# Performance work log

Hardware: AMD Instinct MI355X
Metric: run time of the kernel (lower is better)

## Reference

```python
import jax, jax.numpy as jnp
import numpy as np

B, L, C, D, H, NB, K = 8, 1024, 4, 64, 8, 2, 16  # batch, seq, conds, dim, heads, blocks, rbf centers

def _ln(x, s, b):
    m = x.mean(-1, keepdims=True)
    v = x.var(-1, keepdims=True)
    return (x - m) / jnp.sqrt(v + 1e-6) * s + b

def setup_inputs() -> dict:
    key = jax.random.key(0)
    ks = jax.random.split(key, 24)
    rn = lambda i, shape, sc=0.02: jax.random.normal(ks[i], shape, jnp.float32) * sc
    inp = {}
    inp['z'] = jax.random.normal(ks[0], (B, L), jnp.float32)
    inp['conditionals'] = jax.random.normal(ks[1], (C,), jnp.float32)
    inp['s'] = jnp.sort(jax.random.uniform(ks[2], (L,), jnp.float32))
    inp['embed'] = rn(3, (L, 2 * D - (C + 1)))  # positional id embedding table
    # input MLP([4D, D]) with gelu
    inp['Win1'] = rn(4, (2 * D, 4 * D)); inp['bin1'] = jnp.zeros((4 * D,), jnp.float32)
    inp['Win2'] = rn(5, (4 * D, D));     inp['bin2'] = jnp.zeros((D,), jnp.float32)
    # per-block (leading dim NB) transformer params
    inp['ln1_s'] = jnp.ones((NB, D), jnp.float32); inp['ln1_b'] = jnp.zeros((NB, D), jnp.float32)
    inp['ln2_s'] = jnp.ones((NB, D), jnp.float32); inp['ln2_b'] = jnp.zeros((NB, D), jnp.float32)
    inp['Wq'] = rn(6, (NB, D, 2 * D)); inp['bq'] = jnp.zeros((NB, 2 * D), jnp.float32)
    inp['Wk'] = rn(7, (NB, D, 2 * D)); inp['bk'] = jnp.zeros((NB, 2 * D), jnp.float32)
    inp['Wv'] = rn(8, (NB, D, 2 * D)); inp['bv'] = jnp.zeros((NB, 2 * D), jnp.float32)
    inp['Wo'] = rn(9, (NB, 2 * D, D)); inp['bo'] = jnp.zeros((NB, D), jnp.float32)
    # RBF-network attention bias: features exp(-(d-c)^2/(2w^2)) -> linear to H heads
    inp['rbf_c'] = jnp.tile(jnp.linspace(-1.0, 1.0, K, dtype=jnp.float32)[None], (NB, 1))
    inp['rbf_logw'] = jnp.full((NB, K), -1.0, jnp.float32)
    inp['rbf_w'] = rn(10, (NB, K, H), 0.1); inp['rbf_b'] = jnp.zeros((NB, H), jnp.float32)
    # FFN MLP([4D, D])
    inp['W1'] = rn(11, (NB, D, 4 * D)); inp['b1'] = jnp.zeros((NB, 4 * D), jnp.float32)
    inp['W2'] = rn(12, (NB, 4 * D, D)); inp['b2'] = jnp.zeros((NB, D), jnp.float32)
    # head MLP([4D, D, 1])
    inp['Wh1'] = rn(13, (D, 4 * D)); inp['bh1'] = jnp.zeros((4 * D,), jnp.float32)
    inp['Wh2'] = rn(14, (4 * D, D)); inp['bh2'] = jnp.zeros((D,), jnp.float32)
    inp['Wh3'] = rn(15, (D, 1));     inp['bh3'] = jnp.zeros((1,), jnp.float32)
    return inp

def reference(z, conditionals, s, embed, Win1, bin1, Win2, bin2,
              ln1_s, ln1_b, ln2_s, ln2_b, Wq, bq, Wk, bk, Wv, bv, Wo, bo,
              rbf_c, rbf_logw, rbf_w, rbf_b, W1, b1, W2, b2,
              Wh1, bh1, Wh2, bh2, Wh3, bh3):
    Bn, Ln = z.shape
    Cn = conditionals.shape[0]
    Hn = rbf_w.shape[-1]
    dh = Wq.shape[-1] // Hn
    scale = 1.0 / jnp.sqrt(jnp.float32(dh))
    # cond_as_feats: [z, broadcast conditionals] -> (B, L, C+1); prepend ids embedding -> (B, L, 2D)
    feats = jnp.concatenate([
        jnp.broadcast_to(embed[None], (Bn,) + embed.shape),
        z[..., None],
        jnp.broadcast_to(conditionals[None, None, :], (Bn, Ln, Cn)),
    ], axis=-1)
    x = jax.nn.gelu(feats @ Win1 + bin1) @ Win2 + bin2  # (B, L, D)
    dist = s[:, None] - s[None, :]  # (L, L) pairwise query-key coordinate diff (same per batch)
    for i in range(Wq.shape[0]):
        h = _ln(x, ln1_s[i], ln1_b[i])
        q = (h @ Wq[i] + bq[i]).reshape(Bn, Ln, Hn, dh)
        k = (h @ Wk[i] + bk[i]).reshape(Bn, Ln, Hn, dh)
        v = (h @ Wv[i] + bv[i]).reshape(Bn, Ln, Hn, dh)
        scores = jnp.einsum('bqhd,bkhd->bhqk', q, k) * scale
        # RBF-network bias on pairwise distances, per head
        phi = jnp.exp(-(dist[..., None] - rbf_c[i]) ** 2 / (2.0 * jnp.exp(rbf_logw[i]) ** 2))  # (L, L, K)
        bias = jnp.einsum('qkf,fh->hqk', phi, rbf_w[i]) + rbf_b[i][:, None, None]  # (H, L, L)
        a = jax.nn.softmax(scores + bias[None], axis=-1)
        o = jnp.einsum('bhqk,bkhd->bqhd', a, v).reshape(Bn, Ln, Hn * dh)
        x = x + o @ Wo[i] + bo[i]
        h2 = _ln(x, ln2_s[i], ln2_b[i])
        x = x + jax.nn.gelu(h2 @ W1[i] + b1[i]) @ W2[i] + b2[i]
    hh = jax.nn.gelu(x @ Wh1 + bh1)
    hh = jax.nn.gelu(hh @ Wh2 + bh2)
    return hh @ Wh3 + bh3  # f_hat: (B, L, 1)
```

## Files before the change

### kernel.cpp

```cpp
#include <hip/hip_runtime.h>
#include <hip/hip_bf16.h>

#define BB   8
#define LL   1024
#define DD   64
#define D2   128
#define D4   256
#define HH   8
#define DH   16

typedef __attribute__((ext_vector_type(8))) short short8;
typedef __attribute__((ext_vector_type(4))) float floatx4;

#define LOG2E 1.4426950408889634f
#define QK_SEED -66.54214054f

#define OB_QUAR 1048576
#define L_QUAR  65536

#define OFF_WIN1   0
#define OFF_WIN2   65536
#define OFF_LAY0   98304
#define LAY_STRIDE 131072
#define OFF_WQ     0
#define OFF_WK     16384
#define OFF_WV     32768
#define OFF_WO     49152
#define OFF_W1     65536
#define OFF_W2     98304
#define OFF_WH1    360448
#define OFF_WH2    393216

__device__ __forceinline__ float gelu_tanh(float u) {
  float y = 0.7978845608028654f * (u + 0.044715f * u * u * u);
  return __fdividef(u, 1.0f + __expf(-2.0f * y));
}

__device__ __forceinline__ float wave_reduce_sum(float v) {
#pragma unroll
  for (int m = 32; m >= 1; m >>= 1) v += __shfl_xor(v, m, 64);
  return v;
}

__device__ __forceinline__ unsigned short f2bf(float x) {
  unsigned u = __float_as_uint(x);
  u += 0x7fffu + ((u >> 16) & 1u);
  return (unsigned short)(u >> 16);
}

__device__ __forceinline__ float bf2f(unsigned short x) {
  return __uint_as_float(((unsigned)x) << 16);
}

__device__ __forceinline__ void split_bf(float v, unsigned short& hi,
                                         unsigned short& lo) {
  hi = f2bf(v);
  lo = f2bf(v - bf2f(hi));
}

__device__ __forceinline__ unsigned pack_bf2(float a, float b) {
  unsigned ua = __float_as_uint(a) + 0x8000u;
  unsigned ub = __float_as_uint(b) + 0x8000u;
  return __builtin_amdgcn_perm(ub, ua, 0x07060302u);
}

__device__ __forceinline__ int frag_off(int k, int n, int K) {
  return (n >> 4) * (K * 16) + ((k >> 5) << 9) + (((k >> 3) & 3) << 7) +
         ((n & 15) << 3) + (k & 7);
}

template <int K, int KP>
__device__ __forceinline__ floatx4 mfma_tile(
    const unsigned short* Ah, const unsigned short* Al,
    const unsigned short* __restrict__ Bf, const unsigned short* __restrict__ Bfl,
    int lane, int lq, int quad, floatx4 C) {
  floatx4 C1 = {0.0f, 0.0f, 0.0f, 0.0f};
  floatx4 C2 = {0.0f, 0.0f, 0.0f, 0.0f};
#pragma unroll
  for (int kk = 0; kk < K; kk += 32) {
    short8 ah = *(const short8*)(Ah + lq * KP + kk + quad * 8);
    short8 al = *(const short8*)(Al + lq * KP + kk + quad * 8);
    short8 bh = *(const short8*)(Bf + (kk >> 5) * 512 + lane * 8);
    short8 bl = *(const short8*)(Bfl + (kk >> 5) * 512 + lane * 8);
    C  = __builtin_amdgcn_mfma_f32_16x16x32_bf16(ah, bh, C, 0, 0, 0);
    C1 = __builtin_amdgcn_mfma_f32_16x16x32_bf16(al, bh, C1, 0, 0, 0);
    C2 = __builtin_amdgcn_mfma_f32_16x16x32_bf16(ah, bl, C2, 0, 0, 0);
  }
#pragma unroll
  for (int r = 0; r < 4; ++r) C[r] += C1[r] + C2[r];
  return C;
}

struct PrepArgs {
  const float* src[16];
  int Kd[16], Nd[16], dst[16], elems[16];
};

__global__ __launch_bounds__(256) void k_prep_bias(
    PrepArgs a, unsigned short* __restrict__ arena,
    const float* __restrict__ s, const float* __restrict__ rbf_c,
    const float* __restrict__ rbf_logw, const float* __restrict__ rbf_w,
    const float* __restrict__ rbf_b, unsigned short* __restrict__ biasT) {
  int bid = blockIdx.x, t = threadIdx.x;
  if (bid < 2048) {
    int mid = bid >> 7;
    int e = (bid & 127) * 256 + t;
    int KN = a.elems[mid];
    if (e >= KN) return;
    int K = a.Kd[mid], N = a.Nd[mid];
    int n = e / K, k = e - n * K;
    float wv = a.src[mid][k * N + n];
    unsigned short hi, lo;
    split_bf(wv, hi, lo);
    int fo = frag_off(k, n, K);
    arena[a.dst[mid] + fo] = hi;
    arena[a.dst[mid] + KN + fo] = lo;
    return;
  }
  __shared__ float cs[16], iw[16];
  int rem = bid - 2048;
  int lay = rem >> 12;
  if (t < 16) {
    cs[t] = rbf_c[lay * 16 + t];
    iw[t] = 0.5f * __expf(-2.0f * rbf_logw[lay * 16 + t]);
  }
  __syncthreads();
  int id = (rem & 4095) * 256 + t;
  int q = id >> 10, k = id & 1023;
  float dd = s[q] - s[k];
  float acc[8];
#pragma unroll
  for (int h = 0; h < 8; ++h) acc[h] = rbf_b[lay * 8 + h];
#pragma unroll 1
  for (int f = 0; f < 16; ++f) {
    float e = dd - cs[f];
    float ph = __expf(-e * e * iw[f]);
#pragma unroll
    for (int h = 0; h < 8; ++h)
      acc[h] = fmaf(ph, rbf_w[lay * 128 + f * 8 + h], acc[h]);
  }
  unsigned short* bT = biasT + (size_t)lay * 8 * 1024 * 1024;
#pragma unroll
  for (int h = 0; h < 8; ++h)
    bT[(size_t)(h * 1024 + q) * 1024 + k] = f2bf(acc[h] * LOG2E);
}

__device__ __forceinline__ void qkv_tail(
    const float* xl, unsigned short* Sh, unsigned short* Sl,
    const unsigned short* __restrict__ arena, int lay,
    const float* __restrict__ ln_s, const float* __restrict__ ln_b,
    const float* __restrict__ bq, const float* __restrict__ bk,
    const float* __restrict__ bv, unsigned short* __restrict__ qo,
    unsigned short* __restrict__ ko, unsigned short* __restrict__ voT,
    int tok0, int t) {
  int w = t >> 6, lane = t & 63;
  int lq = lane & 15, quad = lane >> 4;
  float ss = ln_s[lay * 64 + lane], sb = ln_b[lay * 64 + lane];
#pragma unroll
  for (int tk = 0; tk < 4; ++tk) {
    int tok = w * 4 + tk;
    float v = xl[tok * 64 + lane];
    float s1 = v, s2 = v * v;
#pragma unroll
    for (int m = 32; m >= 1; m >>= 1) {
      s1 += __shfl_xor(s1, m, 64);
      s2 += __shfl_xor(s2, m, 64);
    }
    float mean = s1 * 0.015625f;
    float var = fmaf(-mean, mean, s2 * 0.015625f);
    float hv = (v - mean) * rsqrtf(var + 1e-6f) * ss + sb;
    unsigned short hi, lo;
    split_bf(hv, hi, lo);
    Sh[tok * 72 + lane] = hi;
    Sl[tok * 72 + lane] = lo;
  }
  __syncthreads();
  int b = tok0 >> 10, l0 = tok0 & 1023;
#pragma unroll 1
  for (int mat = 0; mat < 3; ++mat) {
    const unsigned short* Bh =
        arena + OFF_LAY0 + lay * LAY_STRIDE + mat * 16384;
    const unsigned short* Bl = Bh + 8192;
    const float* bias = (mat == 0 ? bq : mat == 1 ? bk : bv) + lay * 128;
#pragma unroll
    for (int j = 0; j < 2; ++j) {
      int tl = w + j * 4;
      int n = tl * 16 + lq;
      float bb = bias[n];
      floatx4 C = {bb, bb, bb, bb};
      C = mfma_tile<64, 72>(Sh, Sl, Bh + tl * 16 * 64, Bl + tl * 16 * 64,
                            lane, lq, quad, C);
      if (mat < 2) {
        unsigned short* outp = (mat == 0 ? qo : ko);
        size_t basea = ((size_t)(b * 8 + tl) * 1024 + l0 + quad * 4) * 16 + lq;
#pragma unroll
        for (int r = 0; r < 4; ++r)
          outp[basea + (size_t)r * 16] = f2bf(C[r]);
      } else {
        size_t basev = ((size_t)(b * 8 + tl) * 16 + lq) * 1024 + l0 + quad * 4;
#pragma unroll
        for (int r = 0; r < 4; ++r)
          voT[basev + r] = f2bf(C[r]);
      }
    }
  }
}

__global__ __launch_bounds__(256, 2) void k_in_qkv(
    const float* __restrict__ embed, const float* __restrict__ z,
    const float* __restrict__ cond, const unsigned short* __restrict__ arena,
    const float* __restrict__ bin1, const float* __restrict__ bin2,
    float* __restrict__ x, const float* __restrict__ ln1_s,
    const float* __restrict__ ln1_b, const float* __restrict__ bq,
    const float* __restrict__ bk, const float* __restrict__ bv,
    unsigned short* __restrict__ qo, unsigned short* __restrict__ ko,
    unsigned short* __restrict__ voT) {
  __shared__ __align__(16) unsigned short Ah[16 * 136], Al[16 * 136];
  __shared__ __align__(16) unsigned short Hh[16 * 264], Hl[16 * 264];
  __shared__ __align__(16) unsigned short Sh[16 * 72], Sl[16 * 72];
  __shared__ float xl[16 * 64];
  int t = threadIdx.x, w = t >> 6, lane = t & 63;
  int lq = lane & 15, quad = lane >> 4;
  int tok0 = blockIdx.x * 16;
  for (int idx = t; idx < 2048; idx += 256) {
    int tok = idx >> 7, dim = idx & 127;
    int bl = tok0 + tok, l = bl & (LL - 1);
    float v;
    if (dim < 123) v = embed[l * 123 + dim];
    else if (dim == 123) v = z[bl];
    else v = cond[dim - 124];
    unsigned short hi, lo;
    split_bf(v, hi, lo);
    Ah[tok * 136 + dim] = hi;
    Al[tok * 136 + dim] = lo;
  }
  __syncthreads();
  const unsigned short* B1h = arena + OFF_WIN1;
  const unsigned short* B1l = B1h + 32768;
#pragma unroll
  for (int j = 0; j < 4; ++j) {
    int tl = w * 4 + j, n = tl * 16 + lq;
    float bb = bin1[n];
    floatx4 C = {bb, bb, bb, bb};
    C = mfma_tile<128, 136>(Ah, Al, B1h + tl * 16 * 128, B1l + tl * 16 * 128,
                            lane, lq, quad, C);
#pragma unroll
    for (int r = 0; r < 4; ++r) {
      float g = gelu_tanh(C[r]);
      unsigned short hi, lo;
      split_bf(g, hi, lo);
      Hh[(quad * 4 + r) * 264 + n] = hi;
      Hl[(quad * 4 + r) * 264 + n] = lo;
    }
  }
  __syncthreads();
  const unsigned short* B2h = arena + OFF_WIN2;
  const unsigned short* B2l = B2h + 16384;
  {
    int n = w * 16 + lq;
    float bb = bin2[n];
    floatx4 C = {bb, bb, bb, bb};
    C = mfma_tile<256, 264>(Hh, Hl, B2h + w * 16 * 256, B2l + w * 16 * 256,
                            lane, lq, quad, C);
#pragma unroll
    for (int r = 0; r < 4; ++r) {
      int m = quad * 4 + r;
      x[(size_t)(tok0 + m) * 64 + n] = C[r];
      xl[m * 64 + n] = C[r];
    }
  }
  __syncthreads();
  qkv_tail(xl, Sh, Sl, arena, 0, ln1_s, ln1_b, bq, bk, bv,
           qo, ko, voT, tok0, t);
}

__global__ __launch_bounds__(256) void k_attn(
    const unsigned short* __restrict__ qg, const unsigned short* __restrict__ kg,
    const unsigned short* __restrict__ vgT, const unsigned short* __restrict__ biasT,
    float* __restrict__ og, float* __restrict__ lsum) {
  __shared__ __align__(16) unsigned short Kl[64 * 40];
  __shared__ __align__(16) unsigned short VT[16 * 72];
  __shared__ __align__(16) unsigned short Pl[4][16 * 72];
  __shared__ __align__(16) unsigned short Bch[64 * 72];
  int t = threadIdx.x, w = t >> 6, lane = t & 63;
  int lq = lane & 15, quad = lane >> 4;
  int bid = blockIdx.x;
  int quarter = bid >> 10;
  int rem = bid & 1023;
  int b = rem >> 7, h = (rem >> 4) & 7, qblk = rem & 15;
  int q0w = qblk * 64 + w * 16;
  int kbase = quarter * 256;
  size_t bh = (size_t)(b * 8 + h) * 1024;
  size_t bh16 = (size_t)(b * 8 + h) * 16;

  ((uint4*)Kl)[t] = uint4{0, 0, 0, 0};
  if (t < 64) ((uint4*)Kl)[256 + t] = uint4{0, 0, 0, 0};

  short8 Qb = {};
  if (quad < 2)
    Qb = *(const short8*)(qg + (bh + q0w + lq) * 16 + quad * 8);

  float l = 0.0f;
  floatx4 O = {0.0f, 0.0f, 0.0f, 0.0f};

  int key = t >> 2, dp = (t & 3) * 4;
  int drow = t >> 4, vcol = (t & 15) * 4;
  int qrow = t >> 2, bcol = (t & 3) * 16;
  const unsigned short* kgp = kg + (bh + kbase + key) * 16 + dp;
  const unsigned short* vgp = vgT + (bh16 + drow) * 1024 + kbase + vcol;
  const unsigned short* bgp =
      biasT + ((size_t)(h * 1024 + qblk * 64 + qrow)) * 1024 + kbase + bcol;

  uint2 kpre = *(const uint2*)(kgp);
  uint2 vpre = *(const uint2*)(vgp);
  uint4 bpre0 = *(const uint4*)(bgp);
  uint4 bpre1 = *(const uint4*)(bgp + 8);

#pragma unroll 1
  for (int kc = 0; kc < 256; kc += 64) {
    __syncthreads();
    *(uint2*)(Kl + key * 40 + dp) = kpre;
    *(uint2*)(VT + drow * 72 + vcol) = vpre;
    *(uint4*)(Bch + qrow * 72 + bcol) = bpre0;
    *(uint4*)(Bch + qrow * 72 + bcol + 8) = bpre1;
    __syncthreads();
    if (kc + 64 < 256) {
      kpre = *(const uint2*)(kgp + (size_t)(kc + 64) * 16);
      vpre = *(const uint2*)(vgp + (kc + 64));
      bpre0 = *(const uint4*)(bgp + (kc + 64));
      bpre1 = *(const uint4*)(bgp + (kc + 64) + 8);
    }
    float psum = 0.0f;
    unsigned short* pw = &Pl[w][lq * 72];
#pragma unroll
    for (int tile = 0; tile < 4; ++tile) {
      short8 A = *(const short8*)(Kl + (tile * 16 + lq) * 40 + quad * 8);
      floatx4 c = {QK_SEED, QK_SEED, QK_SEED, QK_SEED};
      c = __builtin_amdgcn_mfma_f32_16x16x32_bf16(A, Qb, c, 0, 0, 0);
      ushort4 bb = *(const ushort4*)(Bch + (w * 16 + lq) * 72 +
                                     tile * 16 + quad * 4);
      float p0 = exp2f(fmaf(c[0], 0.25f * LOG2E, bf2f(bb.x)));
      float p1 = exp2f(fmaf(c[1], 0.25f * LOG2E, bf2f(bb.y)));
      float p2 = exp2f(fmaf(c[2], 0.25f * LOG2E, bf2f(bb.z)));
      float p3 = exp2f(fmaf(c[3], 0.25f * LOG2E, bf2f(bb.w)));
      psum += (p0 + p1) + (p2 + p3);
      uint2 pk;
      pk.x = pack_bf2(p0, p1);
      pk.y = pack_bf2(p2, p3);
      *(uint2*)(pw + tile * 16 + quad * 4) = pk;
    }
    psum += __shfl_xor(psum, 16, 64);
    psum += __shfl_xor(psum, 32, 64);
    l += psum;
    asm volatile("s_waitcnt lgkmcnt(0)" ::: "memory");
#pragma unroll
    for (int i = 0; i < 2; ++i) {
      short8 Pa = *(const short8*)(pw + i * 32 + quad * 8);
      short8 Vb = *(const short8*)(&VT[lq * 72 + i * 32 + quad * 8]);
      O = __builtin_amdgcn_mfma_f32_16x16x32_bf16(Pa, Vb, O, 0, 0, 0);
    }
  }
  float* ogh = og + (size_t)quarter * OB_QUAR;
#pragma unroll
  for (int r = 0; r < 4; ++r)
    ogh[((size_t)(b * 1024 + q0w + quad * 4 + r)) * 128 + h * 16 + lq] = O[r];
  if (quad == 0)
    lsum[(size_t)quarter * L_QUAR + (size_t)(b * 1024 + q0w + lq) * 8 + h] = l;
}

__device__ __forceinline__ void pf_body(
    const float* __restrict__ ob, const float* __restrict__ lsum,
    const unsigned short* __restrict__ arena,
    const float* __restrict__ bo, float* __restrict__ x,
    const float* __restrict__ ln_s, const float* __restrict__ ln_b,
    const float* __restrict__ b1, const float* __restrict__ b2, int lay,
    unsigned short* Ah, unsigned short* Al, unsigned short* Sh,
    unsigned short* Sl, unsigned short* Hh, unsigned short* Hl, float* xl,
    int tok0, int t, bool write_x) {
  int w = t >> 6, lane = t & 63;
  int lq = lane & 15, quad = lane >> 4;
  const unsigned short* labase = arena + OFF_LAY0 + lay * LAY_STRIDE;
  const float* ob1 = ob + OB_QUAR;
  const float* ob2 = ob + 2 * OB_QUAR;
  const float* ob3 = ob + 3 * OB_QUAR;
  for (int idx = t * 4; idx < 2048; idx += 1024) {
    int row = idx >> 7, col = idx & 127;
    int hh = col >> 4;
    int tok = tok0 + row;
    float lv = ((lsum[(size_t)tok * 8 + hh] +
                 lsum[L_QUAR + (size_t)tok * 8 + hh]) +
                (lsum[2 * L_QUAR + (size_t)tok * 8 + hh] +
                 lsum[3 * L_QUAR + (size_t)tok * 8 + hh]));
    float linv = 1.0f / lv;
    float4 v0 = *(const float4*)(ob + (size_t)tok * 128 + col);
    float4 v1 = *(const float4*)(ob1 + (size_t)tok * 128 + col);
    float4 v2 = *(const float4*)(ob2 + (size_t)tok * 128 + col);
    float4 v3 = *(const float4*)(ob3 + (size_t)tok * 128 + col);
    float4 v;
    v.x = ((v0.x + v1.x) + (v2.x + v3.x)) * linv;
    v.y = ((v0.y + v1.y) + (v2.y + v3.y)) * linv;
    v.z = ((v0.z + v1.z) + (v2.z + v3.z)) * linv;
    v.w = ((v0.w + v1.w) + (v2.w + v3.w)) * linv;
    unsigned short h0, e0, h1, e1, h2, e2, h3, e3;
    split_bf(v.x, h0, e0); split_bf(v.y, h1, e1);
    split_bf(v.z, h2, e2); split_bf(v.w, h3, e3);
    unsigned* ph = (unsigned*)(Ah + row * 136 + col);
    ph[0] = (unsigned)h0 | ((unsigned)h1 << 16);
    ph[1] = (unsigned)h2 | ((unsigned)h3 << 16);
    unsigned* pl = (unsigned*)(Al + row * 136 + col);
    pl[0] = (unsigned)e0 | ((unsigned)e1 << 16);
    pl[1] = (unsigned)e2 | ((unsigned)e3 << 16);
  }
  __syncthreads();
  {
    const unsigned short* Bh = labase + OFF_WO;
    const unsigned short* Bl = Bh + 8192;
    int n = w * 16 + lq;
    float bb = bo[lay * 64 + n];
    floatx4 C = {bb, bb, bb, bb};
    C = mfma_tile<128, 136>(Ah, Al, Bh + w * 16 * 128, Bl + w * 16 * 128,
                            lane, lq, quad, C);
#pragma unroll
    for (int r = 0; r < 4; ++r) {
      int m = quad * 4 + r;
      xl[m * 64 + n] = x[(size_t)(tok0 + m) * 64 + n] + C[r];
    }
  }
  __syncthreads();
  {
    float ss = ln_s[lay * 64 + lane], sb = ln_b[lay * 64 + lane];
#pragma unroll
    for (int tk = 0; tk < 4; ++tk) {
      int tok = w * 4 + tk;
      float v = xl[tok * 64 + lane];
      float s1 = v, s2 = v * v;
#pragma unroll
      for (int m = 32; m >= 1; m >>= 1) {
        s1 += __shfl_xor(s1, m, 64);
        s2 += __shfl_xor(s2, m, 64);
      }
      float mean = s1 * 0.015625f;
      float var = fmaf(-mean, mean, s2 * 0.015625f);
      float hv = (v - mean) * rsqrtf(var + 1e-6f) * ss + sb;
      unsigned short hi, lo;
      split_bf(hv, hi, lo);
      Sh[tok * 72 + lane] = hi;
      Sl[tok * 72 + lane] = lo;
    }
  }
  __syncthreads();
  {
    const unsigned short* Bh = labase + OFF_W1;
    const unsigned short* Bl = Bh + 16384;
#pragma unroll
    for (int j = 0; j < 4; ++j) {
      int tl = w * 4 + j, n = tl * 16 + lq;
      float bb = b1[lay * 256 + n];
      floatx4 C = {bb, bb, bb, bb};
      C = mfma_tile<64, 72>(Sh, Sl, Bh + tl * 16 * 64, Bl + tl * 16 * 64,
                            lane, lq, quad, C);
#pragma unroll
      for (int r = 0; r < 4; ++r) {
        float g = gelu_tanh(C[r]);
        unsigned short hi, lo;
        split_bf(g, hi, lo);
        Hh[(quad * 4 + r) * 264 + n] = hi;
        Hl[(quad * 4 + r) * 264 + n] = lo;
      }
    }
  }
  __syncthreads();
  {
    const unsigned short* Bh = labase + OFF_W2;
    const unsigned short* Bl = Bh + 16384;
    int n = w * 16 + lq;
    float bb = b2[lay * 64 + n];
    floatx4 C = {bb, bb, bb, bb};
    C = mfma_tile<256, 264>(Hh, Hl, Bh + w * 16 * 256, Bl + w * 16 * 256,
                            lane, lq, quad, C);
#pragma unroll
    for (int r = 0; r < 4; ++r) {
      int m = quad * 4 + r;
      float xv = xl[m * 64 + n] + C[r];
      xl[m * 64 + n] = xv;
      if (write_x) x[(size_t)(tok0 + m) * 64 + n] = xv;
    }
  }
  __syncthreads();
}

__global__ __launch_bounds__(256, 2) void k_pf_qkv(
    const float* __restrict__ ob, const float* __restrict__ lsum,
    const unsigned short* __restrict__ arena,
    const float* __restrict__ bo, float* __restrict__ x,
    const float* __restrict__ ln2_s, const float* __restrict__ ln2_b,
    const float* __restrict__ b1, const float* __restrict__ b2, int lay,
    const float* __restrict__ ln1_s, const float* __restrict__ ln1_b,
    const float* __restrict__ bq, const float* __restrict__ bk,
    const float* __restrict__ bv, unsigned short* __restrict__ qo,
    unsigned short* __restrict__ ko, unsigned short* __restrict__ voT) {
  __shared__ __align__(16) unsigned short Ah[16 * 136], Al[16 * 136];
  __shared__ __align__(16) unsigned short Sh[16 * 72], Sl[16 * 72];
  __shared__ __align__(16) unsigned short Hh[16 * 264], Hl[16 * 264];
  __shared__ float xl[16 * 64];
  int t = threadIdx.x;
  int tok0 = blockIdx.x * 16;
  pf_body(ob, lsum, arena, bo, x, ln2_s, ln2_b, b1, b2, lay,
          Ah, Al, Sh, Sl, Hh, Hl, xl, tok0, t, true);
  qkv_tail(xl, Sh, Sl, arena, lay + 1, ln1_s, ln1_b, bq, bk, bv,
           qo, ko, voT, tok0, t);
}

__global__ __launch_bounds__(256, 2) void k_pf_head(
    const float* __restrict__ ob, const float* __restrict__ lsum,
    const unsigned short* __restrict__ arena,
    const float* __restrict__ bo, float* __restrict__ x,
    const float* __restrict__ ln2_s, const float* __restrict__ ln2_b,
    const float* __restrict__ b1, const float* __restrict__ b2, int lay,
    const float* __restrict__ bh1, const float* __restrict__ bh2,
    const float* __restrict__ Wh3, const float* __restrict__ bh3,
    float* __restrict__ out) {
  __shared__ __align__(16) unsigned short Ah[16 * 136], Al[16 * 136];
  __shared__ __align__(16) unsigned short Sh[16 * 72], Sl[16 * 72];
  __shared__ __align__(16) unsigned short Hh[16 * 264], Hl[16 * 264];
  __shared__ float xl[16 * 64];
  int t = threadIdx.x, w = t >> 6, lane = t & 63;
  int lq = lane & 15, quad = lane >> 4;
  int tok0 = blockIdx.x * 16;
  pf_body(ob, lsum, arena, bo, x, ln2_s, ln2_b, b1, b2, lay,
          Ah, Al, Sh, Sl, Hh, Hl, xl, tok0, t, false);
#pragma unroll
  for (int tk = 0; tk < 4; ++tk) {
    int tok = w * 4 + tk;
    unsigned short hi, lo;
    split_bf(xl[tok * 64 + lane], hi, lo);
    Sh[tok * 72 + lane] = hi;
    Sl[tok * 72 + lane] = lo;
  }
  __syncthreads();
  {
    const unsigned short* Bh = arena + OFF_WH1;
    const unsigned short* Bl = Bh + 16384;
#pragma unroll
    for (int j = 0; j < 4; ++j) {
      int tl = w * 4 + j, n = tl * 16 + lq;
      float bb = bh1[n];
      floatx4 C = {bb, bb, bb, bb};
      C = mfma_tile<64, 72>(Sh, Sl, Bh + tl * 16 * 64, Bl + tl * 16 * 64,
                            lane, lq, quad, C);
#pragma unroll
      for (int r = 0; r < 4; ++r) {
        float g = gelu_tanh(C[r]);
        unsigned short hi, lo;
        split_bf(g, hi, lo);
        Hh[(quad * 4 + r) * 264 + n] = hi;
        Hl[(quad * 4 + r) * 264 + n] = lo;
      }
    }
  }
  __syncthreads();
  {
    const unsigned short* Bh = arena + OFF_WH2;
    const unsigned short* Bl = Bh + 16384;
    int n = w * 16 + lq;
    float bb = bh2[n];
    floatx4 C = {bb, bb, bb, bb};
    C = mfma_tile<256, 264>(Hh, Hl, Bh + w * 16 * 256, Bl + w * 16 * 256,
                            lane, lq, quad, C);
    __syncthreads();
#pragma unroll
    for (int r = 0; r < 4; ++r)
      xl[(quad * 4 + r) * 64 + n] = gelu_tanh(C[r]);
  }
  __syncthreads();
  float wv3 = Wh3[lane];
#pragma unroll
  for (int tk = 0; tk < 4; ++tk) {
    int tok = w * 4 + tk;
    float v = xl[tok * 64 + lane] * wv3;
    float sum = wave_reduce_sum(v);
    if (lane == 0) out[tok0 + tok] = sum + bh3[0];
  }
}

extern "C" void kernel_launch(void* const* d_in, const int* in_sizes, int n_in,
                              void* d_out, int out_size, void* d_ws, size_t ws_size,
                              hipStream_t stream) {
  const float* z      = (const float*)d_in[0];
  const float* cond   = (const float*)d_in[1];
  const float* s      = (const float*)d_in[2];
  const float* embed  = (const float*)d_in[3];
  const float* Win1   = (const float*)d_in[4];
  const float* bin1   = (const float*)d_in[5];
  const float* Win2   = (const float*)d_in[6];
  const float* bin2   = (const float*)d_in[7];
  const float* ln1_s  = (const float*)d_in[8];
  const float* ln1_b  = (const float*)d_in[9];
  const float* ln2_s  = (const float*)d_in[10];
  const float* ln2_b  = (const float*)d_in[11];
  const float* Wq     = (const float*)d_in[12];
  const float* bq     = (const float*)d_in[13];
  const float* Wk     = (const float*)d_in[14];
  const float* bk     = (const float*)d_in[15];
  const float* Wv     = (const float*)d_in[16];
  const float* bv     = (const float*)d_in[17];
  const float* Wo     = (const float*)d_in[18];
  const float* bo     = (const float*)d_in[19];
  const float* rbf_c  = (const float*)d_in[20];
  const float* rbf_lw = (const float*)d_in[21];
  const float* rbf_w  = (const float*)d_in[22];
  const float* rbf_b  = (const float*)d_in[23];
  const float* W1     = (const float*)d_in[24];
  const float* b1     = (const float*)d_in[25];
  const float* W2     = (const float*)d_in[26];
  const float* b2     = (const float*)d_in[27];
  const float* Wh1    = (const float*)d_in[28];
  const float* bh1    = (const float*)d_in[29];
  const float* Wh2    = (const float*)d_in[30];
  const float* bh2    = (const float*)d_in[31];
  const float* Wh3    = (const float*)d_in[32];
  const float* bh3    = (const float*)d_in[33];

  char* base = (char*)d_ws;
  float*          x     = (float*)(base);
  unsigned short* qb    = (unsigned short*)(base + (2u << 20));
  unsigned short* kb    = (unsigned short*)(base + (4u << 20));
  unsigned short* vbT   = (unsigned short*)(base + (6u << 20));
  float*          ob    = (float*)(base + (8u << 20));
  float*          lsum  = (float*)(base + (24u << 20));
  unsigned short* biasT = (unsigned short*)(base + (25u << 20));
  unsigned short* arena = (unsigned short*)(base + (57u << 20));

  PrepArgs pa;
  auto set = [&](int i, const float* sp, int K, int N, int dst) {
    pa.src[i] = sp; pa.Kd[i] = K; pa.Nd[i] = N; pa.dst[i] = dst;
    pa.elems[i] = K * N;
  };
  set(0, Win1, 128, 256, OFF_WIN1);
  set(1, Win2, 256, 64, OFF_WIN2);
  for (int lay = 0; lay < 2; ++lay) {
    int lb = OFF_LAY0 + lay * LAY_STRIDE;
    set(2 + lay * 6, Wq + lay * 8192, 64, 128, lb + OFF_WQ);
    set(3 + lay * 6, Wk + lay * 8192, 64, 128, lb + OFF_WK);
    set(4 + lay * 6, Wv + lay * 8192, 64, 128, lb + OFF_WV);
    set(5 + lay * 6, Wo + lay * 8192, 128, 64, lb + OFF_WO);
    set(6 + lay * 6, W1 + lay * 16384, 64, 256, lb + OFF_W1);
    set(7 + lay * 6, W2 + lay * 16384, 256, 64, lb + OFF_W2);
  }
  set(14, Wh1, 64, 256, OFF_WH1);
  set(15, Wh2, 256, 64, OFF_WH2);

  k_prep_bias<<<2048 + 8192, 256, 0, stream>>>(pa, arena, s, rbf_c, rbf_lw,
                                               rbf_w, rbf_b, biasT);
  k_in_qkv<<<512, 256, 0, stream>>>(embed, z, cond, arena, bin1, bin2, x,
                                    ln1_s, ln1_b, bq, bk, bv, qb, kb, vbT);
  k_attn<<<4096, 256, 0, stream>>>(qb, kb, vbT, biasT, ob, lsum);
  k_pf_qkv<<<512, 256, 0, stream>>>(ob, lsum, arena, bo, x, ln2_s, ln2_b,
                                    b1, b2, 0, ln1_s, ln1_b, bq, bk, bv,
                                    qb, kb, vbT);
  k_attn<<<4096, 256, 0, stream>>>(qb, kb, vbT,
                                   biasT + (size_t)8 * 1024 * 1024, ob, lsum);
  k_pf_head<<<512, 256, 0, stream>>>(ob, lsum, arena, bo, x, ln2_s, ln2_b,
                                     b1, b2, 1, bh1, bh2, Wh3, bh3,
                                     (float*)d_out);
}
```

Baseline: 238.6 us.

## Double threads per block in MLP kernels with split-K reduction via LDS

Result: no change. 239.3 us (median of 2 runs) (+0.3%).

```diff
diff --git a/kernel.cpp b/kernel.cpp
--- a/kernel.cpp
+++ b/kernel.cpp
@@ -157,8 +157,8 @@
   int lq = lane & 15, quad = lane >> 4;
   float ss = ln_s[lay * 64 + lane], sb = ln_b[lay * 64 + lane];
 #pragma unroll
-  for (int tk = 0; tk < 4; ++tk) {
-    int tok = w * 4 + tk;
+  for (int tk = 0; tk < 2; ++tk) {
+    int tok = w * 2 + tk;
     float v = xl[tok * 64 + lane];
     float s1 = v, s2 = v * v;
 #pragma unroll
@@ -176,37 +176,34 @@
   }
   __syncthreads();
   int b = tok0 >> 10, l0 = tok0 & 1023;
+  int tl = w;
 #pragma unroll 1
   for (int mat = 0; mat < 3; ++mat) {
     const unsigned short* Bh =
         arena + OFF_LAY0 + lay * LAY_STRIDE + mat * 16384;
     const unsigned short* Bl = Bh + 8192;
     const float* bias = (mat == 0 ? bq : mat == 1 ? bk : bv) + lay * 128;
-#pragma unroll
-    for (int j = 0; j < 2; ++j) {
-      int tl = w + j * 4;
-      int n = tl * 16 + lq;
-      float bb = bias[n];
-      floatx4 C = {bb, bb, bb, bb};
-      C = mfma_tile<64, 72>(Sh, Sl, Bh + tl * 16 * 64, Bl + tl * 16 * 64,
-                            lane, lq, quad, C);
-      if (mat < 2) {
-        unsigned short* outp = (mat == 0 ? qo : ko);
-        size_t basea = ((size_t)(b * 8 + tl) * 1024 + l0 + quad * 4) * 16 + lq;
-#pragma unroll
-        for (int r = 0; r < 4; ++r)
-          outp[basea + (size_t)r * 16] = f2bf(C[r]);
-      } else {
-        size_t basev = ((size_t)(b * 8 + tl) * 16 + lq) * 1024 + l0 + quad * 4;
-#pragma unroll
-        for (int r = 0; r < 4; ++r)
-          voT[basev + r] = f2bf(C[r]);
-      }
-    }
-  }
-}
-
-__global__ __launch_bounds__(256, 2) void k_in_qkv(
+    int n = tl * 16 + lq;
+    float bb = bias[n];
+    floatx4 C = {bb, bb, bb, bb};
+    C = mfma_tile<64, 72>(Sh, Sl, Bh + tl * 16 * 64, Bl + tl * 16 * 64,
+                          lane, lq, quad, C);
+    if (mat < 2) {
+      unsigned short* outp = (mat == 0 ? qo : ko);
+      size_t basea = ((size_t)(b * 8 + tl) * 1024 + l0 + quad * 4) * 16 + lq;
+#pragma unroll
+      for (int r = 0; r < 4; ++r)
+        outp[basea + (size_t)r * 16] = f2bf(C[r]);
+    } else {
+      size_t basev = ((size_t)(b * 8 + tl) * 16 + lq) * 1024 + l0 + quad * 4;
+#pragma unroll
+      for (int r = 0; r < 4; ++r)
+        voT[basev + r] = f2bf(C[r]);
+    }
+  }
+}
+
+__global__ __launch_bounds__(512, 4) void k_in_qkv(
     const float* __restrict__ embed, const float* __restrict__ z,
     const float* __restrict__ cond, const unsigned short* __restrict__ arena,
     const float* __restrict__ bin1, const float* __restrict__ bin2,
@@ -219,10 +216,11 @@
   __shared__ __align__(16) unsigned short Hh[16 * 264], Hl[16 * 264];
   __shared__ __align__(16) unsigned short Sh[16 * 72], Sl[16 * 72];
   __shared__ float xl[16 * 64];
+  __shared__ __align__(16) float red[4 * 64 * 4];
   int t = threadIdx.x, w = t >> 6, lane = t & 63;
   int lq = lane & 15, quad = lane >> 4;
   int tok0 = blockIdx.x * 16;
-  for (int idx = t; idx < 2048; idx += 256) {
+  for (int idx = t; idx < 2048; idx += 512) {
     int tok = idx >> 7, dim = idx & 127;
     int bl = tok0 + tok, l = bl & (LL - 1);
     float v;
@@ -238,8 +236,8 @@
   const unsigned short* B1h = arena + OFF_WIN1;
   const unsigned short* B1l = B1h + 32768;
 #pragma unroll
-  for (int j = 0; j < 4; ++j) {
-    int tl = w * 4 + j, n = tl * 16 + lq;
+  for (int j = 0; j < 2; ++j) {
+    int tl = w * 2 + j, n = tl * 16 + lq;
     float bb = bin1[n];
     floatx4 C = {bb, bb, bb, bb};
     C = mfma_tile<128, 136>(Ah, Al, B1h + tl * 16 * 128, B1l + tl * 16 * 128,
@@ -254,19 +252,31 @@
     }
   }
   __syncthreads();
-  const unsigned short* B2h = arena + OFF_WIN2;
-  const unsigned short* B2l = B2h + 16384;
   {
-    int n = w * 16 + lq;
-    float bb = bin2[n];
-    floatx4 C = {bb, bb, bb, bb};
-    C = mfma_tile<256, 264>(Hh, Hl, B2h + w * 16 * 256, B2l + w * 16 * 256,
+    const unsigned short* B2h = arena + OFF_WIN2;
+    const unsigned short* B2l = B2h + 16384;
+    int tile = w & 3, kh = w >> 2, koff = kh * 128;
+    int n = tile * 16 + lq;
+    floatx4 C = {0.0f, 0.0f, 0.0f, 0.0f};
+    if (kh == 0) {
+      float bb = bin2[n];
+      C[0] = bb; C[1] = bb; C[2] = bb; C[3] = bb;
+    }
+    C = mfma_tile<128, 264>(Hh + koff, Hl + koff,
+                            B2h + tile * 16 * 256 + (koff >> 5) * 512,
+                            B2l + tile * 16 * 256 + (koff >> 5) * 512,
                             lane, lq, quad, C);
-#pragma unroll
-    for (int r = 0; r < 4; ++r) {
-      int m = quad * 4 + r;
-      x[(size_t)(tok0 + m) * 64 + n] = C[r];
-      xl[m * 64 + n] = C[r];
+    if (kh) *(floatx4*)&red[(tile * 64 + lane) * 4] = C;
+    __syncthreads();
+    if (!kh) {
+      floatx4 Cp = *(const floatx4*)&red[(tile * 64 + lane) * 4];
+#pragma unroll
+      for (int r = 0; r < 4; ++r) {
+        int m = quad * 4 + r;
+        float cv = C[r] + Cp[r];
+        x[(size_t)(tok0 + m) * 64 + n] = cv;
+        xl[m * 64 + n] = cv;
+      }
     }
   }
   __syncthreads();
@@ -376,14 +386,15 @@
     const float* __restrict__ b1, const float* __restrict__ b2, int lay,
     unsigned short* Ah, unsigned short* Al, unsigned short* Sh,
     unsigned short* Sl, unsigned short* Hh, unsigned short* Hl, float* xl,
-    int tok0, int t, bool write_x) {
+    float* red, int tok0, int t, bool write_x) {
   int w = t >> 6, lane = t & 63;
   int lq = lane & 15, quad = lane >> 4;
   const unsigned short* labase = arena + OFF_LAY0 + lay * LAY_STRIDE;
   const float* ob1 = ob + OB_QUAR;
   const float* ob2 = ob + 2 * OB_QUAR;
   const float* ob3 = ob + 3 * OB_QUAR;
-  for (int idx = t * 4; idx < 2048; idx += 1024) {
+  {
+    int idx = t * 4;
     int row = idx >> 7, col = idx & 127;
     int hh = col >> 4;
     int tok = tok0 + row;
@@ -415,23 +426,34 @@
   {
     const unsigned short* Bh = labase + OFF_WO;
     const unsigned short* Bl = Bh + 8192;
-    int n = w * 16 + lq;
-    float bb = bo[lay * 64 + n];
-    floatx4 C = {bb, bb, bb, bb};
-    C = mfma_tile<128, 136>(Ah, Al, Bh + w * 16 * 128, Bl + w * 16 * 128,
-                            lane, lq, quad, C);
-#pragma unroll
-    for (int r = 0; r < 4; ++r) {
-      int m = quad * 4 + r;
-      xl[m * 64 + n] = x[(size_t)(tok0 + m) * 64 + n] + C[r];
+    int tile = w & 3, kh = w >> 2, koff = kh * 64;
+    int n = tile * 16 + lq;
+    floatx4 C = {0.0f, 0.0f, 0.0f, 0.0f};
+    if (kh == 0) {
+      float bb = bo[lay * 64 + n];
+      C[0] = bb; C[1] = bb; C[2] = bb; C[3] = bb;
+    }
+    C = mfma_tile<64, 136>(Ah + koff, Al + koff,
+                           Bh + tile * 16 * 128 + (koff >> 5) * 512,
+                           Bl + tile * 16 * 128 + (koff >> 5) * 512,
+                           lane, lq, quad, C);
+    if (kh) *(floatx4*)&red[(tile * 64 + lane) * 4] = C;
+    __syncthreads();
+    if (!kh) {
+      floatx4 Cp = *(const floatx4*)&red[(tile * 64 + lane) * 4];
+#pragma unroll
+      for (int r = 0; r < 4; ++r) {
+        int m = quad * 4 + r;
+        xl[m * 64 + n] = x[(size_t)(tok0 + m) * 64 + n] + C[r] + Cp[r];
+      }
     }
   }
   __syncthreads();
   {
     float ss = ln_s[lay * 64 + lane], sb = ln_b[lay * 64 + lane];
 #pragma unroll
-    for (int tk = 0; tk < 4; ++tk) {
-      int tok = w * 4 + tk;
+    for (int tk = 0; tk < 2; ++tk) {
+      int tok = w * 2 + tk;
       float v = xl[tok * 64 + lane];
       float s1 = v, s2 = v * v;
 #pragma unroll
@@ -453,8 +475,8 @@
     const unsigned short* Bh = labase + OFF_W1;
     const unsigned short* Bl = Bh + 16384;
 #pragma unroll
-    for (int j = 0; j < 4; ++j) {
-      int tl = w * 4 + j, n = tl * 16 + lq;
+    for (int j = 0; j < 2; ++j) {
+      int tl = w * 2 + j, n = tl * 16 + lq;
       float bb = b1[lay * 256 + n];
       floatx4 C = {bb, bb, bb, bb};
       C = mfma_tile<64, 72>(Sh, Sl, Bh + tl * 16 * 64, Bl + tl * 16 * 64,
@@ -473,23 +495,34 @@
   {
     const unsigned short* Bh = labase + OFF_W2;
     const unsigned short* Bl = Bh + 16384;
-    int n = w * 16 + lq;
-    float bb = b2[lay * 64 + n];
-    floatx4 C = {bb, bb, bb, bb};
-    C = mfma_tile<256, 264>(Hh, Hl, Bh + w * 16 * 256, Bl + w * 16 * 256,
+    int tile = w & 3, kh = w >> 2, koff = kh * 128;
+    int n = tile * 16 + lq;
+    floatx4 C = {0.0f, 0.0f, 0.0f, 0.0f};
+    if (kh == 0) {
+      float bb = b2[lay * 64 + n];
+      C[0] = bb; C[1] = bb; C[2] = bb; C[3] = bb;
+    }
+    C = mfma_tile<128, 264>(Hh + koff, Hl + koff,
+                            Bh + tile * 16 * 256 + (koff >> 5) * 512,
+                            Bl + tile * 16 * 256 + (koff >> 5) * 512,
                             lane, lq, quad, C);
-#pragma unroll
-    for (int r = 0; r < 4; ++r) {
-      int m = quad * 4 + r;
-      float xv = xl[m * 64 + n] + C[r];
-      xl[m * 64 + n] = xv;
-      if (write_x) x[(size_t)(tok0 + m) * 64 + n] = xv;
-    }
-  }
-  __syncthreads();
-}
-
-__global__ __launch_bounds__(256, 2) void k_pf_qkv(
+    if (kh) *(floatx4*)&red[(tile * 64 + lane) * 4] = C;
+    __syncthreads();
+    if (!kh) {
+      floatx4 Cp = *(const floatx4*)&red[(tile * 64 + lane) * 4];
+#pragma unroll
+      for (int r = 0; r < 4; ++r) {
+        int m = quad * 4 + r;
+        float xv = xl[m * 64 + n] + C[r] + Cp[r];
+        xl[m * 64 + n] = xv;
+        if (write_x) x[(size_t)(tok0 + m) * 64 + n] = xv;
+      }
+    }
+  }
+  __syncthreads();
+}
+
+__global__ __launch_bounds__(512, 4) void k_pf_qkv(
     const float* __restrict__ ob, const float* __restrict__ lsum,
     const unsigned short* __restrict__ arena,
     const float* __restrict__ bo, float* __restrict__ x,
@@ -503,15 +536,16 @@
   __shared__ __align__(16) unsigned short Sh[16 * 72], Sl[16 * 72];
   __shared__ __align__(16) unsigned short Hh[16 * 264], Hl[16 * 264];
   __shared__ float xl[16 * 64];
+  __shared__ __align__(16) float red[4 * 64 * 4];
   int t = threadIdx.x;
   int tok0 = blockIdx.x * 16;
   pf_body(ob, lsum, arena, bo, x, ln2_s, ln2_b, b1, b2, lay,
-          Ah, Al, Sh, Sl, Hh, Hl, xl, tok0, t, true);
+          Ah, Al, Sh, Sl, Hh, Hl, xl, red, tok0, t, true);
   qkv_tail(xl, Sh, Sl, arena, lay + 1, ln1_s, ln1_b, bq, bk, bv,
            qo, ko, voT, tok0, t);
 }
 
-__global__ __launch_bounds__(256, 2) void k_pf_head(
+__global__ __launch_bounds__(512, 4) void k_pf_head(
     const float* __restrict__ ob, const float* __restrict__ lsum,
     const unsigned short* __restrict__ arena,
     const float* __restrict__ bo, float* __restrict__ x,
@@ -524,14 +558,15 @@
   __shared__ __align__(16) unsigned short Sh[16 * 72], Sl[16 * 72];
   __shared__ __align__(16) unsigned short Hh[16 * 264], Hl[16 * 264];
   __shared__ float xl[16 * 64];
+  __shared__ __align__(16) float red[4 * 64 * 4];
   int t = threadIdx.x, w = t >> 6, lane = t & 63;
   int lq = lane & 15, quad = lane >> 4;
   int tok0 = blockIdx.x * 16;
   pf_body(ob, lsum, arena, bo, x, ln2_s, ln2_b, b1, b2, lay,
-          Ah, Al, Sh, Sl, Hh, Hl, xl, tok0, t, false);
-#pragma unroll
-  for (int tk = 0; tk < 4; ++tk) {
-    int tok = w * 4 + tk;
+          Ah, Al, Sh, Sl, Hh, Hl, xl, red, tok0, t, false);
+#pragma unroll
+  for (int tk = 0; tk < 2; ++tk) {
+    int tok = w * 2 + tk;
     unsigned short hi, lo;
     split_bf(xl[tok * 64 + lane], hi, lo);
     Sh[tok * 72 + lane] = hi;
@@ -542,8 +577,8 @@
     const unsigned short* Bh = arena + OFF_WH1;
     const unsigned short* Bl = Bh + 16384;
 #pragma unroll
-    for (int j = 0; j < 4; ++j) {
-      int tl = w * 4 + j, n = tl * 16 + lq;
+    for (int j = 0; j < 2; ++j) {
+      int tl = w * 2 + j, n = tl * 16 + lq;
       float bb = bh1[n];
       floatx4 C = {bb, bb, bb, bb};
       C = mfma_tile<64, 72>(Sh, Sl, Bh + tl * 16 * 64, Bl + tl * 16 * 64,
@@ -562,21 +597,31 @@
   {
     const unsigned short* Bh = arena + OFF_WH2;
     const unsigned short* Bl = Bh + 16384;
-    int n = w * 16 + lq;
-    float bb = bh2[n];
-    floatx4 C = {bb, bb, bb, bb};
-    C = mfma_tile<256, 264>(Hh, Hl, Bh + w * 16 * 256, Bl + w * 16 * 256,
+    int tile = w & 3, kh = w >> 2, koff = kh * 128;
+    int n = tile * 16 + lq;
+    floatx4 C = {0.0f, 0.0f, 0.0f, 0.0f};
+    if (kh == 0) {
+      float bb = bh2[n];
+      C[0] = bb; C[1] = bb; C[2] = bb; C[3] = bb;
+    }
+    C = mfma_tile<128, 264>(Hh + koff, Hl + koff,
+                            Bh + tile * 16 * 256 + (koff >> 5) * 512,
+                            Bl + tile * 16 * 256 + (koff >> 5) * 512,
                             lane, lq, quad, C);
+    if (kh) *(floatx4*)&red[(tile * 64 + lane) * 4] = C;
     __syncthreads();
-#pragma unroll
-    for (int r = 0; r < 4; ++r)
-      xl[(quad * 4 + r) * 64 + n] = gelu_tanh(C[r]);
+    if (!kh) {
+      floatx4 Cp = *(const floatx4*)&red[(tile * 64 + lane) * 4];
+#pragma unroll
+      for (int r = 0; r < 4; ++r)
+        xl[(quad * 4 + r) * 64 + n] = gelu_tanh(C[r] + Cp[r]);
+    }
   }
   __syncthreads();
   float wv3 = Wh3[lane];
 #pragma unroll
-  for (int tk = 0; tk < 4; ++tk) {
-    int tok = w * 4 + tk;
+  for (int tk = 0; tk < 2; ++tk) {
+    int tok = w * 2 + tk;
     float v = xl[tok * 64 + lane] * wv3;
     float sum = wave_reduce_sum(v);
     if (lane == 0) out[tok0 + tok] = sum + bh3[0];
@@ -652,15 +697,15 @@
 
   k_prep_bias<<<2048 + 8192, 256, 0, stream>>>(pa, arena, s, rbf_c, rbf_lw,
                                                rbf_w, rbf_b, biasT);
-  k_in_qkv<<<512, 256, 0, stream>>>(embed, z, cond, arena, bin1, bin2, x,
+  k_in_qkv<<<512, 512, 0, stream>>>(embed, z, cond, arena, bin1, bin2, x,
                                     ln1_s, ln1_b, bq, bk, bv, qb, kb, vbT);
   k_attn<<<4096, 256, 0, stream>>>(qb, kb, vbT, biasT, ob, lsum);
-  k_pf_qkv<<<512, 256, 0, stream>>>(ob, lsum, arena, bo, x, ln2_s, ln2_b,
+  k_pf_qkv<<<512, 512, 0, stream>>>(ob, lsum, arena, bo, x, ln2_s, ln2_b,
                                     b1, b2, 0, ln1_s, ln1_b, bq, bk, bv,
                                     qb, kb, vbT);
   k_attn<<<4096, 256, 0, stream>>>(qb, kb, vbT,
                                    biasT + (size_t)8 * 1024 * 1024, ob, lsum);
-  k_pf_head<<<512, 256, 0, stream>>>(ob, lsum, arena, bo, x, ln2_s, ln2_b,
+  k_pf_head<<<512, 512, 0, stream>>>(ob, lsum, arena, bo, x, ln2_s, ln2_b,
                                      b1, b2, 1, bh1, bh2, Wh3, bh3,
                                      (float*)d_out);
 }
```
